# Performance work log

Measured on AMD Instinct MI355X. Metric: run time of the kernel, lower is better.

The kernel has to match this reference:

```python
import jax, jax.numpy as jnp
import numpy as np

HEADS = 8
DIM_HEAD = 64
MAX_POS = 512


def setup_inputs() -> dict:
    key = jax.random.key(0)
    ks = jax.random.split(key, 10)
    b, n, dim, inner = 4, 1024, 512, HEADS * DIM_HEAD
    w = lambda k, shape: jax.random.normal(k, shape, jnp.float32) * 0.02
    return {
        "x": jax.random.normal(ks[0], (b, n, dim, 2), jnp.float32),
        "wq_r": w(ks[1], (dim, inner)),
        "wq_i": w(ks[2], (dim, inner)),
        "wkv_r": w(ks[3], (dim, 2 * inner)),
        "wkv_i": w(ks[4], (dim, 2 * inner)),
        "wo_r": w(ks[5], (inner, dim)),
        "wo_i": w(ks[6], (inner, dim)),
        "bo_r": w(ks[7], (dim,)),
        "bo_i": w(ks[8], (dim,)),
        "rel_emb": w(ks[9], (2 * MAX_POS + 1, DIM_HEAD)),
    }


def _clinear(t, Wr, Wi, br=None, bi=None):
    # complex linear: (a+ib)(Wr+iWi) = (aWr - bWi) + i(bWr + aWi)
    a, b = t[..., 0], t[..., 1]
    r = a @ Wr - b @ Wi
    i = b @ Wr + a @ Wi
    if br is not None:
        r = r + br
        i = i + bi
    return jnp.stack((r, i), axis=-1)


def _split_heads(t, h):
    # [b, n, h*d, 2] -> [b, h, n, d, 2]
    b, n, hd, c = t.shape
    return t.reshape(b, n, h, hd // h, c).transpose(0, 2, 1, 3, 4)


def reference(x, wq_r, wq_i, wkv_r, wkv_i, wo_r, wo_i, bo_r, bo_i, rel_emb):
    b, n = x.shape[0], x.shape[1]
    scale = DIM_HEAD ** (-0.5)

    q = _split_heads(_clinear(x, wq_r, wq_i), HEADS)          # [b,h,n,d,2]
    kv = _clinear(x, wkv_r, wkv_i)                            # [b,n,2*inner,2]
    k_, v_ = jnp.split(kv, 2, axis=-2)
    k = _split_heads(k_, HEADS)
    v = _split_heads(v_, HEADS)

    qr, qi = q[..., 0], q[..., 1]
    kr, ki = k[..., 0], k[..., 1]

    dots_r = (jnp.einsum('bhid,bhjd->bhij', qr, kr)
              - jnp.einsum('bhid,bhjd->bhij', qi, ki)) * scale
    dots_i = (jnp.einsum('bhid,bhjd->bhij', qr, ki)
              + jnp.einsum('bhid,bhjd->bhij', qi, kr)) * scale

    seq = jnp.arange(n)
    dist = jnp.clip(seq[:, None] - seq[None, :], -MAX_POS, MAX_POS) + MAX_POS  # [n,n]
    rel = rel_emb[dist]                                       # [n, n, d]
    dots_r = dots_r + jnp.einsum('bhnd,nrd->bhnr', qr, rel) * scale
    dots_i = dots_i + jnp.einsum('bhnd,nrd->bhnr', qi, rel) * scale

    # magnitude softmax over keys
    attn = jax.nn.softmax(jnp.sqrt(dots_r ** 2 + dots_i ** 2), axis=-1)  # [b,h,i,j]

    vr, vi = v[..., 0], v[..., 1]
    out_r = jnp.einsum('bhij,bhjd->bhid', attn, vr)
    out_i = jnp.einsum('bhij,bhjd->bhid', attn, vi)
    # [b,h,n,d] -> [b,n,h*d]
    out_r = out_r.transpose(0, 2, 1, 3).reshape(b, n, -1)
    out_i = out_i.transpose(0, 2, 1, 3).reshape(b, n, -1)
    out = jnp.stack((out_r, out_i), axis=-1)                  # [b,n,inner,2]

    # to_out (with bias); dropout prob 0 -> identity
    return _clinear(out, wo_r, wo_i, bo_r, bo_i)
```

## Files before the change

kernel.cpp:

```cpp
#include <hip/hip_runtime.h>
#include <hip/hip_bf16.h>


using bf16 = __bf16;
typedef __bf16 bf16x8 __attribute__((ext_vector_type(8)));
typedef float f32x4 __attribute__((ext_vector_type(4)));
typedef unsigned u32x4 __attribute__((ext_vector_type(4)));

#define MFMA16(a, b, c) __builtin_amdgcn_mfma_f32_16x16x32_bf16((a), (b), (c), 0, 0, 0)

__device__ __forceinline__ float ld_in(const void* p, long long i, int f32) {
  return f32 ? ((const float*)p)[i] : (float)((const bf16*)p)[i];
}

__device__ __forceinline__ void gl_lds16(const bf16* g, const bf16* l) {
  __builtin_amdgcn_global_load_lds(
      (const __attribute__((address_space(1))) void*)(unsigned long long)g,
      (__attribute__((address_space(3))) void*)(unsigned int)(unsigned long long)l,
      16, 0, 0);
}

template <int CTRL>
__device__ __forceinline__ float dpp_mv(float v) {
  int s = __builtin_bit_cast(int, v);
  return __builtin_bit_cast(float,
      __builtin_amdgcn_update_dpp(s, s, CTRL, 0xf, 0xf, false));
}
__device__ __forceinline__ float dpp_sum16(float v) {
  v += dpp_mv<0x121>(v);
  v += dpp_mv<0x122>(v);
  v += dpp_mv<0x124>(v);
  v += dpp_mv<0x128>(v);
  return v;
}

__device__ __forceinline__ unsigned pack_bf16(float lo, float hi) {
  unsigned a = (unsigned)__builtin_bit_cast(unsigned short, (bf16)lo);
  unsigned b = (unsigned)__builtin_bit_cast(unsigned short, (bf16)hi);
  return a | (b << 16);
}
__device__ __forceinline__ unsigned pack2h(bf16 lo, bf16 hi) {
  unsigned a = (unsigned)__builtin_bit_cast(unsigned short, lo);
  unsigned b = (unsigned)__builtin_bit_cast(unsigned short, hi);
  return a | (b << 16);
}

__global__ __launch_bounds__(256) void k_diag(float* __restrict__ out, float v) {
  int idx = blockIdx.x * 256 + threadIdx.x;
  if (idx < 4194304) out[idx] = v;
}

__global__ void k_detect_all(
    const unsigned short* p0, const unsigned short* p1, const unsigned short* p2,
    const unsigned short* p3, const unsigned short* p4, const unsigned short* p5,
    const unsigned short* p6, const unsigned short* p7, const unsigned short* p8,
    const unsigned short* p9, int* __restrict__ flags) {
  static const int sizes[10] = {65536, 65536, 65536, 65536, 65536,
                                65536, 65536, 512, 512, 65536};
  const unsigned short* ptrs[10] = {p0, p1, p2, p3, p4, p5, p6, p7, p8, p9};
  __shared__ int cnt;
  if (threadIdx.x == 0) cnt = 0;
  __syncthreads();
  const int which = blockIdx.x;
  const unsigned short* p = ptrs[which];
  const int nhalf = sizes[which];
  const int ns = nhalf < 4096 ? nhalf : 4096;
  const int stp = nhalf / ns;
  int c = 0;
  for (int i = threadIdx.x; i < ns; i += 256) {
    const unsigned u = p[(size_t)i * stp];
    const unsigned e = (u >> 7) & 0xFF;
    if (e == 0xFF || (e < 64 && (u & 0x7FFF) != 0)) ++c;
  }
  atomicAdd(&cnt, c);
  __syncthreads();
  if (threadIdx.x == 0) flags[which] = (cnt > (ns >> 6)) ? 1 : 0;
}

__global__ __launch_bounds__(256) void k_build_all(
    const void* __restrict__ x,
    const void* __restrict__ wq_r, const void* __restrict__ wq_i,
    const void* __restrict__ wkv_r, const void* __restrict__ wkv_i,
    const void* __restrict__ wo_r, const void* __restrict__ wo_i,
    const void* __restrict__ rel,
    bf16* __restrict__ wct, bf16* __restrict__ wot,
    bf16* __restrict__ xd, bf16* __restrict__ rel_c,
    const int* __restrict__ flags) {
  __shared__ float tile[64][65];
  const int bid = blockIdx.x;
  const int t = threadIdx.x;
  if (bid < 1024) {
    const bool is_o = bid >= 768;
    const int lb = is_o ? bid - 768 : bid;
    const int k0 = (lb & 15) * 64;
    const int c0 = (lb >> 4) * 64;
    const int kk0 = k0 & 511;
    const bool hi = k0 >= 512;
    const void* src;
    int f, ld, scol;
    float sgn = 1.f;
    if (is_o) {
      ld = 512;
      if (c0 < 512) { scol = c0;       if (!hi) { src = wo_r; f = flags[5]; } else { src = wo_i; f = flags[6]; sgn = -1.f; } }
      else          { scol = c0 - 512; if (!hi) { src = wo_i; f = flags[6]; } else { src = wo_r; f = flags[5]; } }
    } else {
      if (c0 < 512)       { scol = c0;        ld = 512;  if (!hi) { src = wq_r;  f = flags[1]; } else { src = wq_i;  f = flags[2]; sgn = -1.f; } }
      else if (c0 < 1024) { scol = c0 - 512;  ld = 512;  if (!hi) { src = wq_i;  f = flags[2]; } else { src = wq_r;  f = flags[1]; } }
      else if (c0 < 2048) { scol = c0 - 1024; ld = 1024; if (!hi) { src = wkv_r; f = flags[3]; } else { src = wkv_i; f = flags[4]; sgn = -1.f; } }
      else                { scol = c0 - 2048; ld = 1024; if (!hi) { src = wkv_i; f = flags[4]; } else { src = wkv_r; f = flags[3]; } }
    }
    const int cc = t & 63, rq = t >> 6;
#pragma unroll
    for (int rp = 0; rp < 16; ++rp) {
      const int rr = rp * 4 + rq;
      tile[rr][cc] = sgn * ld_in(src, (long long)(kk0 + rr) * ld + scol + cc, f);
    }
    __syncthreads();
    bf16* dst = is_o ? wot : wct;
    const int cr = t >> 3, kb = (t & 7) * 8;
#pragma unroll
    for (int p = 0; p < 2; ++p) {
      const int c = cr + p * 32;
      bf16x8 v;
#pragma unroll
      for (int e = 0; e < 8; ++e) v[e] = (bf16)tile[kb + e][c];
      *(bf16x8*)(dst + (size_t)(c0 + c) * 1024 + k0 + kb) = v;
    }
  } else if (bid < 9216) {
    const int f = flags[0];
    int idx = (bid - 1024) * 256 + t;
    int m = idx >> 9, j = idx & 511;
    long long base = (long long)m * 1024 + j * 2;
    xd[(size_t)m * 1024 + j] = (bf16)ld_in(x, base, f);
    xd[(size_t)m * 1024 + 512 + j] = (bf16)ld_in(x, base + 1, f);
  } else {
    const int f = flags[9];
    int idx = (bid - 9216) * 256 + t;
    if (idx < 65600) rel_c[idx] = (bf16)ld_in(rel, idx, f);
  }
}

template <int MODE, int BN>
__global__ __launch_bounds__(256) void k_gemm(
    const bf16* __restrict__ A, const bf16* __restrict__ Bt,
    bf16* __restrict__ C, float* __restrict__ Cf,
    const int M, const int N, const int K,
    const void* __restrict__ bias_r, const void* __restrict__ bias_i,
    const int* __restrict__ flags) {
  constexpr int MT = (BN == 128) ? 4 : 2;
  __shared__ __align__(16) bf16 As[128 * 32];
  __shared__ __align__(16) bf16 Bs[BN * 32];
  const int tid = threadIdx.x;
  const int wave = tid >> 6, lane = tid & 63;
  const int lane15 = lane & 15, quad = lane >> 4;
  const int qk0 = quad * 8;
  const int per = gridDim.x >> 3;
  const int s = (blockIdx.x & 7) * per + (blockIdx.x >> 3);
  const int nbx = N / BN;
  const int bm = (s / nbx) * 128, bn = (s % nbx) * BN;
  int wm, wn;
  if constexpr (BN == 128) { wm = (wave >> 1) * 64; wn = (wave & 1) * 64; }
  else                     { wm = wave * 32;        wn = 0; }
  const int sr = lane >> 2;
  const int sc = (lane & 3) * 8;
  f32x4 acc[MT][4];
#pragma unroll
  for (int i = 0; i < MT; ++i)
#pragma unroll
    for (int j = 0; j < 4; ++j) acc[i][j] = (f32x4){0.f, 0.f, 0.f, 0.f};

  for (int k0 = 0; k0 < K; k0 += 32) {
#pragma unroll
    for (int p = 0; p < 2; ++p) {
      const int r0 = p * 64 + wave * 16;
      gl_lds16(A + (size_t)(bm + r0 + sr) * K + k0 + sc, As + r0 * 32);
    }
    if constexpr (BN == 128) {
#pragma unroll
      for (int p = 0; p < 2; ++p) {
        const int r0 = p * 64 + wave * 16;
        gl_lds16(Bt + (size_t)(bn + r0 + sr) * K + k0 + sc, Bs + r0 * 32);
      }
    } else {
      const int r0 = wave * 16;
      gl_lds16(Bt + (size_t)(bn + r0 + sr) * K + k0 + sc, Bs + r0 * 32);
    }
    __syncthreads();
    bf16x8 af[MT], bfr[4];
#pragma unroll
    for (int mt = 0; mt < MT; ++mt) af[mt] = *(const bf16x8*)(As + (wm + mt * 16 + lane15) * 32 + qk0);
#pragma unroll
    for (int nt = 0; nt < 4; ++nt) bfr[nt] = *(const bf16x8*)(Bs + (wn + nt * 16 + lane15) * 32 + qk0);
#pragma unroll
    for (int mt = 0; mt < MT; ++mt)
#pragma unroll
      for (int nt = 0; nt < 4; ++nt) acc[mt][nt] = MFMA16(af[mt], bfr[nt], acc[mt][nt]);
    __syncthreads();
  }
  int fbr = 0, fbi = 0;
  if constexpr (MODE == 1) { fbr = flags[7]; fbi = flags[8]; }
#pragma unroll
  for (int mt = 0; mt < MT; ++mt)
#pragma unroll
    for (int nt = 0; nt < 4; ++nt)
#pragma unroll
      for (int r = 0; r < 4; ++r) {
        const int m = bm + wm + mt * 16 + quad * 4 + r;
        const int n = bn + wn + nt * 16 + lane15;
        float v = acc[mt][nt][r];
        if constexpr (MODE == 0) {
          C[(size_t)m * N + n] = (bf16)v;
        } else {
          const int c = (n < 512) ? n : n - 512;
          v += ld_in((n < 512) ? bias_r : bias_i, c, (n < 512) ? fbr : fbi);
          Cf[(size_t)m * 1024 + c * 2 + ((n < 512) ? 0 : 1)] = v;
        }
      }
}

__global__ __launch_bounds__(256) void k_vt(const bf16* __restrict__ C1,
                                            bf16* __restrict__ vt_r, bf16* __restrict__ vt_i) {
  __shared__ __align__(16) bf16 tr[64][72], ti[64][72];
  const int bid = blockIdx.x, tid = threadIdx.x;
  const int bh = bid >> 4, jt = bid & 15;
  const int b = bh >> 3, h = bh & 7;
  const int j0 = jt * 64;
#pragma unroll
  for (int p = 0; p < 2; ++p) {
    const int j = p * 32 + (tid >> 3);
    const int d0 = (tid & 7) * 8;
    const size_t base = (size_t)(b * 1024 + j0 + j) * 3072 + h * 64 + d0;
    *(bf16x8*)&tr[j][d0] = *(const bf16x8*)(C1 + base + 1536);
    *(bf16x8*)&ti[j][d0] = *(const bf16x8*)(C1 + base + 2560);
  }
  __syncthreads();
#pragma unroll
  for (int p = 0; p < 2; ++p) {
    const int d = p * 32 + (tid >> 3);
    const int p0 = (tid & 7) * 4;
    u32x4 wr, wi;
#pragma unroll
    for (int e = 0; e < 4; ++e) {
      const int pp = p0 + e;
      const int j1 = ((pp >> 4) << 5) + (pp & 15);
      wr[e] = pack2h(tr[j1][d], tr[j1 + 16][d]);
      wi[e] = pack2h(ti[j1][d], ti[j1 + 16][d]);
    }
    const size_t dst = (size_t)(bh * 64 + d) * 512 + jt * 32 + p0;
    *(u32x4*)((unsigned*)vt_r + dst) = wr;
    *(u32x4*)((unsigned*)vt_i + dst) = wi;
  }
}

__device__ __forceinline__ bf16x8 lds_frag72(const bf16* base, int row, int kofs) {
  return *(const bf16x8*)(base + row * 72 + kofs);
}

__global__ __launch_bounds__(256, 2) void k_attn(
    const bf16* __restrict__ C1, const bf16* __restrict__ vt_r, const bf16* __restrict__ vt_i,
    const bf16* __restrict__ rel, bf16* __restrict__ Oc) {
  __shared__ __align__(16) bf16 kr_s[64 * 72];
  __shared__ __align__(16) bf16 ki_s[64 * 72];
  __shared__ __align__(16) bf16 vtr_s[64 * 72];
  __shared__ __align__(16) bf16 vti_s[64 * 72];
  __shared__ unsigned Gt32[4][1360];

  const int tid = threadIdx.x;
  const int wave = tid >> 6, lane = tid & 63;
  const int lane15 = lane & 15, quad = lane >> 4;
  const int qk0 = quad * 8;
  const int bid0 = blockIdx.x;
  const int bid = (bid0 & 7) * 64 + (bid0 >> 3);
  const int bh = bid >> 4, it = bid & 15;
  const int b = bh >> 3, h = bh & 7;
  const int i0 = it * 64;
  const int tq = tid >> 3;
  const int tc = (tid & 7) * 8;

  unsigned* const Gw = &Gt32[wave][0];

  const size_t qbase = (size_t)(b * 1024 + i0 + wave * 16 + lane15) * 3072 + h * 64;
  bf16x8 aqr[2], aqi[2], aqin[2];
  aqr[0] = *(const bf16x8*)(C1 + qbase + qk0);
  aqr[1] = *(const bf16x8*)(C1 + qbase + 32 + qk0);
  aqi[0] = *(const bf16x8*)(C1 + qbase + 512 + qk0);
  aqi[1] = *(const bf16x8*)(C1 + qbase + 512 + 32 + qk0);
#pragma unroll
  for (int c = 0; c < 2; ++c)
#pragma unroll
    for (int e = 0; e < 8; ++e) aqin[c][e] = (bf16)(-(float)aqi[c][e]);

  f32x4 o_r[4], o_i[4];
#pragma unroll
  for (int dt = 0; dt < 4; ++dt) { o_r[dt] = (f32x4){0.f,0.f,0.f,0.f}; o_i[dt] = (f32x4){0.f,0.f,0.f,0.f}; }
  float l_st[4] = {0.f, 0.f, 0.f, 0.f};

  bf16x8 pKr[2], pKi[2], pVr[2], pVi[2];
  auto issueKV = [&](int jtn) {
    const int j0 = jtn * 64;
#pragma unroll
    for (int p = 0; p < 2; ++p) {
      const int row = p * 32 + tq;
      const size_t gbase = (size_t)(b * 1024 + j0 + row) * 3072 + h * 64 + tc;
      pKr[p] = *(const bf16x8*)(C1 + gbase + 1024);
      pKi[p] = *(const bf16x8*)(C1 + gbase + 2048);
      const size_t vbase = (size_t)(bh * 64 + row) * 1024 + j0 + tc;
      pVr[p] = *(const bf16x8*)(vt_r + vbase);
      pVi[p] = *(const bf16x8*)(vt_i + vbase);
    }
  };

  bf16x8 rb0[5], rb1[5];
  auto loadR = [&](int jtn) {
    const int t0w = 449 + i0 - jtn * 64 + wave * 16;
#pragma unroll
    for (int g = 0; g < 5; ++g) {
      int trw = t0w + g * 16 + lane15;
      trw = trw < 0 ? 0 : (trw > 1024 ? 1024 : trw);
      const bf16* rp = rel + (size_t)trw * 64;
      rb0[g] = *(const bf16x8*)(rp + qk0);
      rb1[g] = *(const bf16x8*)(rp + 32 + qk0);
    }
  };

  issueKV(0);
  loadR(0);
  for (int jt = 0; jt < 16; ++jt) {
#pragma unroll
    for (int p = 0; p < 2; ++p) {
      const int row = p * 32 + tq;
      *(bf16x8*)(kr_s + row * 72 + tc) = pKr[p];
      *(bf16x8*)(ki_s + row * 72 + tc) = pKi[p];
      *(bf16x8*)(vtr_s + row * 72 + tc) = pVr[p];
      *(bf16x8*)(vti_s + row * 72 + tc) = pVi[p];
    }
    __syncthreads();
    if (jt < 15) issueKV(jt + 1);

    f32x4 s_r[4], s_i[4];
#pragma unroll
    for (int ct = 0; ct < 4; ++ct) { s_r[ct] = (f32x4){0.f,0.f,0.f,0.f}; s_i[ct] = (f32x4){0.f,0.f,0.f,0.f}; }
    __builtin_amdgcn_s_setprio(1);
#pragma unroll
    for (int ct = 0; ct < 4; ++ct) {
      const int krow = ct * 16 + lane15;
      bf16x8 bkr0 = lds_frag72(kr_s, krow, qk0), bkr1 = lds_frag72(kr_s, krow, 32 + qk0);
      bf16x8 bki0 = lds_frag72(ki_s, krow, qk0), bki1 = lds_frag72(ki_s, krow, 32 + qk0);
      s_r[ct] = MFMA16(aqr[0], bkr0, s_r[ct]);
      s_r[ct] = MFMA16(aqr[1], bkr1, s_r[ct]);
      s_r[ct] = MFMA16(aqin[0], bki0, s_r[ct]);
      s_r[ct] = MFMA16(aqin[1], bki1, s_r[ct]);
      s_i[ct] = MFMA16(aqr[0], bki0, s_i[ct]);
      s_i[ct] = MFMA16(aqr[1], bki1, s_i[ct]);
      s_i[ct] = MFMA16(aqi[0], bkr0, s_i[ct]);
      s_i[ct] = MFMA16(aqi[1], bkr1, s_i[ct]);
    }
    __builtin_amdgcn_s_setprio(0);

#pragma unroll
    for (int g = 0; g < 5; ++g) {
      f32x4 gr = (f32x4){0.f,0.f,0.f,0.f}, gi = (f32x4){0.f,0.f,0.f,0.f};
      gr = MFMA16(aqr[0], rb0[g], gr);
      gr = MFMA16(aqr[1], rb1[g], gr);
      gi = MFMA16(aqi[0], rb0[g], gi);
      gi = MFMA16(aqi[1], rb1[g], gi);
      const int trow = (g * 16 + lane15) * 17;
#pragma unroll
      for (int r = 0; r < 4; ++r)
        Gw[trow + quad * 4 + r] = pack_bf16(gr[r], gi[r]);
    }

    if (jt < 15) loadR(jt + 1);

    float mag[4][4];
#pragma unroll
    for (int ct = 0; ct < 4; ++ct) {
      const int jj = ct * 16 + lane15;
#pragma unroll
      for (int r = 0; r < 4; ++r) {
        const int ii = quad * 4 + r;
        const unsigned gv = Gw[(ii - jj + 63) * 17 + ii];
        const float gr = __builtin_bit_cast(float, gv << 16);
        const float gi = __builtin_bit_cast(float, gv & 0xffff0000u);
        const float dr = s_r[ct][r] + gr;
        const float di = s_i[ct][r] + gi;
        mag[ct][r] = fminf(0.125f * sqrtf(dr * dr + di * di), 80.f);
      }
    }
#pragma unroll
    for (int r = 0; r < 4; ++r) {
      const int ii = quad * 4 + r;
      float pv[4];
#pragma unroll
      for (int ct = 0; ct < 4; ++ct) pv[ct] = __expf(mag[ct][r]);
      l_st[r] += (pv[0] + pv[1]) + (pv[2] + pv[3]);
      Gw[ii * 36 + lane15]      = pack_bf16(pv[0], pv[1]);
      Gw[ii * 36 + 16 + lane15] = pack_bf16(pv[2], pv[3]);
    }

    bf16x8 ap0 = *(const bf16x8*)(Gw + lane15 * 36 + quad * 4);
    bf16x8 ap1 = *(const bf16x8*)(Gw + lane15 * 36 + 16 + quad * 4);
    __builtin_amdgcn_s_setprio(1);
#pragma unroll
    for (int dt = 0; dt < 4; ++dt) {
      const int vrow = dt * 16 + lane15;
      bf16x8 bv0 = lds_frag72(vtr_s, vrow, qk0), bv1 = lds_frag72(vtr_s, vrow, 32 + qk0);
      o_r[dt] = MFMA16(ap0, bv0, o_r[dt]);
      o_r[dt] = MFMA16(ap1, bv1, o_r[dt]);
      bv0 = lds_frag72(vti_s, vrow, qk0);
      bv1 = lds_frag72(vti_s, vrow, 32 + qk0);
      o_i[dt] = MFMA16(ap0, bv0, o_i[dt]);
      o_i[dt] = MFMA16(ap1, bv1, o_i[dt]);
    }
    __builtin_amdgcn_s_setprio(0);
    __syncthreads();
  }

  const size_t obase = (size_t)(b * 1024 + i0 + wave * 16) * 1024 + h * 64;
#pragma unroll
  for (int r = 0; r < 4; ++r) {
    const float inv = 1.0f / dpp_sum16(l_st[r]);
    const int ii = quad * 4 + r;
#pragma unroll
    for (int dt = 0; dt < 4; ++dt) {
      Oc[obase + (size_t)ii * 1024 + dt * 16 + lane15] = (bf16)(o_r[dt][r] * inv);
      Oc[obase + (size_t)ii * 1024 + 512 + dt * 16 + lane15] = (bf16)(o_i[dt][r] * inv);
    }
  }
}

extern "C" void kernel_launch(void* const* d_in, const int* in_sizes, int n_in,
                              void* d_out, int out_size, void* d_ws, size_t ws_size,
                              hipStream_t stream) {
  float* out = (float*)d_out;

  if (n_in != 10) { k_diag<<<16384, 256, 0, stream>>>(out, 300000.f); return; }
  if (out_size != 4194304) { k_diag<<<16384, 256, 0, stream>>>(out, 400000.f); return; }
  static const int dict_sizes[10] = {4194304, 262144, 262144, 524288, 524288,
                                     262144, 262144, 512, 512, 65600};
  for (int i = 0; i < 10; ++i) {
    if (in_sizes[i] != dict_sizes[i]) { k_diag<<<16384, 256, 0, stream>>>(out, 200000.f); return; }
  }
  const size_t NEED = 50462888;
  if (ws_size < NEED) { k_diag<<<16384, 256, 0, stream>>>(out, 100000.f); return; }

  const void* x     = d_in[0];
  const void* wq_r  = d_in[1];
  const void* wq_i  = d_in[2];
  const void* wkv_r = d_in[3];
  const void* wkv_i = d_in[4];
  const void* wo_r  = d_in[5];
  const void* wo_i  = d_in[6];
  const void* bo_r  = d_in[7];
  const void* bo_i  = d_in[8];
  const void* rel   = d_in[9];

  char* ws = (char*)d_ws;
  bf16* C1   = (bf16*)(ws);
  bf16* Xd   = (bf16*)(ws + 25165824);
  bf16* Vtr  = (bf16*)(ws + 25165824);
  bf16* Vti  = (bf16*)(ws + 29360128);
  bf16* Oc   = (bf16*)(ws + 33554432);
  bf16* WcT  = (bf16*)(ws + 41943040);
  bf16* WoT  = (bf16*)(ws + 48234496);
  bf16* relc = (bf16*)(ws + 50331648);
  int*  flags= (int*)(ws + 50462848);

  k_detect_all<<<10, 256, 0, stream>>>(
      (const unsigned short*)x, (const unsigned short*)wq_r, (const unsigned short*)wq_i,
      (const unsigned short*)wkv_r, (const unsigned short*)wkv_i, (const unsigned short*)wo_r,
      (const unsigned short*)wo_i, (const unsigned short*)bo_r, (const unsigned short*)bo_i,
      (const unsigned short*)rel, flags);

  k_build_all<<<9473, 256, 0, stream>>>(x, wq_r, wq_i, wkv_r, wkv_i, wo_r, wo_i, rel,
                                        WcT, WoT, Xd, relc, flags);

  k_gemm<0, 128><<<768, 256, 0, stream>>>(Xd, WcT, C1, nullptr, 4096, 3072, 1024,
                                          nullptr, nullptr, flags);
  k_vt<<<512, 256, 0, stream>>>(C1, Vtr, Vti);
  k_attn<<<512, 256, 0, stream>>>(C1, Vtr, Vti, relc, Oc);
  k_gemm<1, 64><<<512, 256, 0, stream>>>(Oc, WoT, nullptr, out, 4096, 1024, 1024,
                                         bo_r, bo_i, flags);
}
```

Baseline: 238.6 us.

## Split attention key loop across two wave groups and load V fragments from global

The attention block grows to 512 threads, with two groups of four waves. Each group handles alternating 64-key tiles for the same query rows, and the partial outputs and row sums are combined through LDS at the end. V fragments are now read directly from global memory into registers instead of being staged in shared memory, which cuts LDS traffic and footprint. This doubles the waves per query tile and adds a final reduction. The direct global V reads may hurt latency hiding, and the larger block may change occupancy.

```diff
diff --git a/kernel.cpp b/kernel.cpp
--- a/kernel.cpp
+++ b/kernel.cpp
@@ -256,17 +256,17 @@
   return *(const bf16x8*)(base + row * 72 + kofs);
 }
 
-__global__ __launch_bounds__(256, 2) void k_attn(
+__global__ __launch_bounds__(512, 4) void k_attn(
     const bf16* __restrict__ C1, const bf16* __restrict__ vt_r, const bf16* __restrict__ vt_i,
     const bf16* __restrict__ rel, bf16* __restrict__ Oc) {
-  __shared__ __align__(16) bf16 kr_s[64 * 72];
-  __shared__ __align__(16) bf16 ki_s[64 * 72];
-  __shared__ __align__(16) bf16 vtr_s[64 * 72];
-  __shared__ __align__(16) bf16 vti_s[64 * 72];
-  __shared__ unsigned Gt32[4][1360];
+  __shared__ __align__(16) bf16 k_s[2][2][64 * 72];
+  __shared__ unsigned Gt32[8][1360];
 
   const int tid = threadIdx.x;
-  const int wave = tid >> 6, lane = tid & 63;
+  const int wave = tid >> 6;
+  const int grp = wave >> 2;
+  const int w4 = wave & 3;
+  const int lane = tid & 63;
   const int lane15 = lane & 15, quad = lane >> 4;
   const int qk0 = quad * 8;
   const int bid0 = blockIdx.x;
@@ -274,12 +274,15 @@
   const int bh = bid >> 4, it = bid & 15;
   const int b = bh >> 3, h = bh & 7;
   const int i0 = it * 64;
-  const int tq = tid >> 3;
-  const int tc = (tid & 7) * 8;
+  const int tid256 = tid & 255;
+  const int tq = tid256 >> 3;
+  const int tc = (tid256 & 7) * 8;
 
   unsigned* const Gw = &Gt32[wave][0];
-
-  const size_t qbase = (size_t)(b * 1024 + i0 + wave * 16 + lane15) * 3072 + h * 64;
+  bf16* const krs = &k_s[grp][0][0];
+  bf16* const kis = &k_s[grp][1][0];
+
+  const size_t qbase = (size_t)(b * 1024 + i0 + w4 * 16 + lane15) * 3072 + h * 64;
   bf16x8 aqr[2], aqi[2], aqin[2];
   aqr[0] = *(const bf16x8*)(C1 + qbase + qk0);
   aqr[1] = *(const bf16x8*)(C1 + qbase + 32 + qk0);
@@ -293,10 +296,10 @@
   f32x4 o_r[4], o_i[4];
 #pragma unroll
   for (int dt = 0; dt < 4; ++dt) { o_r[dt] = (f32x4){0.f,0.f,0.f,0.f}; o_i[dt] = (f32x4){0.f,0.f,0.f,0.f}; }
-  float l_st[4] = {0.f, 0.f, 0.f, 0.f};
-
-  bf16x8 pKr[2], pKi[2], pVr[2], pVi[2];
-  auto issueKV = [&](int jtn) {
+  f32x4 l_st = (f32x4){0.f, 0.f, 0.f, 0.f};
+
+  bf16x8 pKr[2], pKi[2];
+  auto issueK = [&](int jtn) {
     const int j0 = jtn * 64;
 #pragma unroll
     for (int p = 0; p < 2; ++p) {
@@ -304,15 +307,12 @@
       const size_t gbase = (size_t)(b * 1024 + j0 + row) * 3072 + h * 64 + tc;
       pKr[p] = *(const bf16x8*)(C1 + gbase + 1024);
       pKi[p] = *(const bf16x8*)(C1 + gbase + 2048);
-      const size_t vbase = (size_t)(bh * 64 + row) * 1024 + j0 + tc;
-      pVr[p] = *(const bf16x8*)(vt_r + vbase);
-      pVi[p] = *(const bf16x8*)(vt_i + vbase);
     }
   };
 
   bf16x8 rb0[5], rb1[5];
   auto loadR = [&](int jtn) {
-    const int t0w = 449 + i0 - jtn * 64 + wave * 16;
+    const int t0w = 449 + i0 - jtn * 64 + w4 * 16;
 #pragma unroll
     for (int g = 0; g < 5; ++g) {
       int trw = t0w + g * 16 + lane15;
@@ -323,19 +323,26 @@
     }
   };
 
-  issueKV(0);
-  loadR(0);
-  for (int jt = 0; jt < 16; ++jt) {
+  issueK(grp);
+  loadR(grp);
+  for (int k = 0; k < 8; ++k) {
+    const int jt = 2 * k + grp;
 #pragma unroll
     for (int p = 0; p < 2; ++p) {
       const int row = p * 32 + tq;
-      *(bf16x8*)(kr_s + row * 72 + tc) = pKr[p];
-      *(bf16x8*)(ki_s + row * 72 + tc) = pKi[p];
-      *(bf16x8*)(vtr_s + row * 72 + tc) = pVr[p];
-      *(bf16x8*)(vti_s + row * 72 + tc) = pVi[p];
+      *(bf16x8*)(krs + row * 72 + tc) = pKr[p];
+      *(bf16x8*)(kis + row * 72 + tc) = pKi[p];
     }
     __syncthreads();
-    if (jt < 15) issueKV(jt + 1);
+    if (k < 7) issueK(2 * (k + 1) + grp);
+
+    bf16x8 vr0[4], vr1[4];
+#pragma unroll
+    for (int dt = 0; dt < 4; ++dt) {
+      const size_t vb = (size_t)(bh * 64 + dt * 16 + lane15) * 1024 + jt * 64;
+      vr0[dt] = *(const bf16x8*)(vt_r + vb + qk0);
+      vr1[dt] = *(const bf16x8*)(vt_r + vb + 32 + qk0);
+    }
 
     f32x4 s_r[4], s_i[4];
 #pragma unroll
@@ -344,8 +351,8 @@
 #pragma unroll
     for (int ct = 0; ct < 4; ++ct) {
       const int krow = ct * 16 + lane15;
-      bf16x8 bkr0 = lds_frag72(kr_s, krow, qk0), bkr1 = lds_frag72(kr_s, krow, 32 + qk0);
-      bf16x8 bki0 = lds_frag72(ki_s, krow, qk0), bki1 = lds_frag72(ki_s, krow, 32 + qk0);
+      bf16x8 bkr0 = lds_frag72(krs, krow, qk0), bkr1 = lds_frag72(krs, krow, 32 + qk0);
+      bf16x8 bki0 = lds_frag72(kis, krow, qk0), bki1 = lds_frag72(kis, krow, 32 + qk0);
       s_r[ct] = MFMA16(aqr[0], bkr0, s_r[ct]);
       s_r[ct] = MFMA16(aqr[1], bkr1, s_r[ct]);
       s_r[ct] = MFMA16(aqin[0], bki0, s_r[ct]);
@@ -357,6 +364,14 @@
     }
     __builtin_amdgcn_s_setprio(0);
 
+    bf16x8 vi0[4], vi1[4];
+#pragma unroll
+    for (int dt = 0; dt < 4; ++dt) {
+      const size_t vb = (size_t)(bh * 64 + dt * 16 + lane15) * 1024 + jt * 64;
+      vi0[dt] = *(const bf16x8*)(vt_i + vb + qk0);
+      vi1[dt] = *(const bf16x8*)(vt_i + vb + 32 + qk0);
+    }
+
 #pragma unroll
     for (int g = 0; g < 5; ++g) {
       f32x4 gr = (f32x4){0.f,0.f,0.f,0.f}, gi = (f32x4){0.f,0.f,0.f,0.f};
@@ -370,7 +385,7 @@
         Gw[trow + quad * 4 + r] = pack_bf16(gr[r], gi[r]);
     }
 
-    if (jt < 15) loadR(jt + 1);
+    if (k < 7) loadR(2 * (k + 1) + grp);
 
     float mag[4][4];
 #pragma unroll
@@ -398,33 +413,51 @@
       Gw[ii * 36 + 16 + lane15] = pack_bf16(pv[2], pv[3]);
     }
 
-    bf16x8 ap0 = *(const bf16x8*)(Gw + lane15 * 36 + quad * 4);
-    bf16x8 ap1 = *(const bf16x8*)(Gw + lane15 * 36 + 16 + quad * 4);
+    bf16x8 ap0 = *(const bf16x8*)((const bf16*)Gw + lane15 * 72 + quad * 8);
+    bf16x8 ap1 = *(const bf16x8*)((const bf16*)Gw + lane15 * 72 + 32 + quad * 8);
     __builtin_amdgcn_s_setprio(1);
 #pragma unroll
     for (int dt = 0; dt < 4; ++dt) {
-      const int vrow = dt * 16 + lane15;
-      bf16x8 bv0 = lds_frag72(vtr_s, vrow, qk0), bv1 = lds_frag72(vtr_s, vrow, 32 + qk0);
-      o_r[dt] = MFMA16(ap0, bv0, o_r[dt]);
-      o_r[dt] = MFMA16(ap1, bv1, o_r[dt]);
-      bv0 = lds_frag72(vti_s, vrow, qk0);
-      bv1 = lds_frag72(vti_s, vrow, 32 + qk0);
-      o_i[dt] = MFMA16(ap0, bv0, o_i[dt]);
-      o_i[dt] = MFMA16(ap1, bv1, o_i[dt]);
+      o_r[dt] = MFMA16(ap0, vr0[dt], o_r[dt]);
+      o_r[dt] = MFMA16(ap1, vr1[dt], o_r[dt]);
+    }
+#pragma unroll
+    for (int dt = 0; dt < 4; ++dt) {
+      o_i[dt] = MFMA16(ap0, vi0[dt], o_i[dt]);
+      o_i[dt] = MFMA16(ap1, vi1[dt], o_i[dt]);
     }
     __builtin_amdgcn_s_setprio(0);
     __syncthreads();
   }
 
-  const size_t obase = (size_t)(b * 1024 + i0 + wave * 16) * 1024 + h * 64;
-#pragma unroll
-  for (int r = 0; r < 4; ++r) {
-    const float inv = 1.0f / dpp_sum16(l_st[r]);
-    const int ii = quad * 4 + r;
+  float* cb = (float*)&k_s[0][0][0];
+  const int base = tid256 * 36;
+  if (grp == 1) {
 #pragma unroll
     for (int dt = 0; dt < 4; ++dt) {
-      Oc[obase + (size_t)ii * 1024 + dt * 16 + lane15] = (bf16)(o_r[dt][r] * inv);
-      Oc[obase + (size_t)ii * 1024 + 512 + dt * 16 + lane15] = (bf16)(o_i[dt][r] * inv);
+      *(f32x4*)(cb + base + dt * 8) = o_r[dt];
+      *(f32x4*)(cb + base + dt * 8 + 4) = o_i[dt];
+    }
+    *(f32x4*)(cb + base + 32) = l_st;
+  }
+  __syncthreads();
+  if (grp == 0) {
+#pragma unroll
+    for (int dt = 0; dt < 4; ++dt) {
+      o_r[dt] += *(const f32x4*)(cb + base + dt * 8);
+      o_i[dt] += *(const f32x4*)(cb + base + dt * 8 + 4);
+    }
+    l_st += *(const f32x4*)(cb + base + 32);
+    const size_t obase = (size_t)(b * 1024 + i0 + w4 * 16) * 1024 + h * 64;
+#pragma unroll
+    for (int r = 0; r < 4; ++r) {
+      const float inv = 1.0f / dpp_sum16(l_st[r]);
+      const int ii = quad * 4 + r;
+#pragma unroll
+      for (int dt = 0; dt < 4; ++dt) {
+        Oc[obase + (size_t)ii * 1024 + dt * 16 + lane15] = (bf16)(o_r[dt][r] * inv);
+        Oc[obase + (size_t)ii * 1024 + 512 + dt * 16 + lane15] = (bf16)(o_i[dt][r] * inv);
+      }
     }
   }
 }
@@ -478,7 +511,7 @@
   k_gemm<0, 128><<<768, 256, 0, stream>>>(Xd, WcT, C1, nullptr, 4096, 3072, 1024,
                                           nullptr, nullptr, flags);
   k_vt<<<512, 256, 0, stream>>>(C1, Vtr, Vti);
-  k_attn<<<512, 256, 0, stream>>>(C1, Vtr, Vti, relc, Oc);
+  k_attn<<<512, 512, 0, stream>>>(C1, Vtr, Vti, relc, Oc);
   k_gemm<1, 64><<<512, 256, 0, stream>>>(Oc, WoT, nullptr, out, 4096, 1024, 1024,
                                          bo_r, bo_i, flags);
 }
```

Result: slower. 481.0 us (+101.6%).

## Pre-swizzle V into MFMA fragment layout and read directly from global; swizzle GEMM LDS

Applied to the files above, without the earlier changes.

The V-transpose kernel now writes V in an MFMA-fragment-ready order so the attention kernel loads B operands for the PV product straight from global memory into registers, dropping two LDS tiles and their stores. This frees LDS, so occupancy is raised to 3 blocks per CU. The rel-embedding loads are moved into the loop body without prefetch, and the barrier placement changes. The GEMM kernel doubles its K tile to 64 and uses an XOR-swizzled LDS layout to avoid bank conflicts. The risk is more global-load latency exposed in the attention inner loop, since V and rel are no longer prefetched a tile ahead.

```diff
diff --git a/kernel.cpp b/kernel.cpp
--- a/kernel.cpp
+++ b/kernel.cpp
@@ -148,12 +148,11 @@
     const void* __restrict__ bias_r, const void* __restrict__ bias_i,
     const int* __restrict__ flags) {
   constexpr int MT = (BN == 128) ? 4 : 2;
-  __shared__ __align__(16) bf16 As[128 * 32];
-  __shared__ __align__(16) bf16 Bs[BN * 32];
+  __shared__ __align__(16) bf16 As[128 * 64];
+  __shared__ __align__(16) bf16 Bs[BN * 64];
   const int tid = threadIdx.x;
   const int wave = tid >> 6, lane = tid & 63;
   const int lane15 = lane & 15, quad = lane >> 4;
-  const int qk0 = quad * 8;
   const int per = gridDim.x >> 3;
   const int s = (blockIdx.x & 7) * per + (blockIdx.x >> 3);
   const int nbx = N / BN;
@@ -161,40 +160,50 @@
   int wm, wn;
   if constexpr (BN == 128) { wm = (wave >> 1) * 64; wn = (wave & 1) * 64; }
   else                     { wm = wave * 32;        wn = 0; }
-  const int sr = lane >> 2;
-  const int sc = (lane & 3) * 8;
+  const int sr = lane >> 3;
+  const int scs = ((lane & 7) ^ sr) * 8;
+  const int s7 = lane15 & 7;
   f32x4 acc[MT][4];
 #pragma unroll
   for (int i = 0; i < MT; ++i)
 #pragma unroll
     for (int j = 0; j < 4; ++j) acc[i][j] = (f32x4){0.f, 0.f, 0.f, 0.f};
 
-  for (int k0 = 0; k0 < K; k0 += 32) {
-#pragma unroll
-    for (int p = 0; p < 2; ++p) {
-      const int r0 = p * 64 + wave * 16;
-      gl_lds16(A + (size_t)(bm + r0 + sr) * K + k0 + sc, As + r0 * 32);
+  for (int k0 = 0; k0 < K; k0 += 64) {
+#pragma unroll
+    for (int p = 0; p < 4; ++p) {
+      const int g = wave * 4 + p;
+      gl_lds16(A + (size_t)(bm + g * 8 + sr) * K + k0 + scs, As + g * 512);
     }
     if constexpr (BN == 128) {
 #pragma unroll
-      for (int p = 0; p < 2; ++p) {
-        const int r0 = p * 64 + wave * 16;
-        gl_lds16(Bt + (size_t)(bn + r0 + sr) * K + k0 + sc, Bs + r0 * 32);
+      for (int p = 0; p < 4; ++p) {
+        const int g = wave * 4 + p;
+        gl_lds16(Bt + (size_t)(bn + g * 8 + sr) * K + k0 + scs, Bs + g * 512);
       }
     } else {
-      const int r0 = wave * 16;
-      gl_lds16(Bt + (size_t)(bn + r0 + sr) * K + k0 + sc, Bs + r0 * 32);
+#pragma unroll
+      for (int p = 0; p < 2; ++p) {
+        const int g = wave * 2 + p;
+        gl_lds16(Bt + (size_t)(bn + g * 8 + sr) * K + k0 + scs, Bs + g * 512);
+      }
     }
     __syncthreads();
-    bf16x8 af[MT], bfr[4];
-#pragma unroll
-    for (int mt = 0; mt < MT; ++mt) af[mt] = *(const bf16x8*)(As + (wm + mt * 16 + lane15) * 32 + qk0);
-#pragma unroll
-    for (int nt = 0; nt < 4; ++nt) bfr[nt] = *(const bf16x8*)(Bs + (wn + nt * 16 + lane15) * 32 + qk0);
-#pragma unroll
-    for (int mt = 0; mt < MT; ++mt)
-#pragma unroll
-      for (int nt = 0; nt < 4; ++nt) acc[mt][nt] = MFMA16(af[mt], bfr[nt], acc[mt][nt]);
+#pragma unroll
+    for (int kk = 0; kk < 2; ++kk) {
+      const int go = ((kk * 4 + quad) ^ s7) * 8;
+      bf16x8 af[MT], bfr[4];
+#pragma unroll
+      for (int mt = 0; mt < MT; ++mt)
+        af[mt] = *(const bf16x8*)(As + (wm + mt * 16 + lane15) * 64 + go);
+#pragma unroll
+      for (int nt = 0; nt < 4; ++nt)
+        bfr[nt] = *(const bf16x8*)(Bs + (wn + nt * 16 + lane15) * 64 + go);
+#pragma unroll
+      for (int mt = 0; mt < MT; ++mt)
+#pragma unroll
+        for (int nt = 0; nt < 4; ++nt) acc[mt][nt] = MFMA16(af[mt], bfr[nt], acc[mt][nt]);
+    }
     __syncthreads();
   }
   int fbr = 0, fbi = 0;
@@ -234,21 +243,21 @@
     *(bf16x8*)&ti[j][d0] = *(const bf16x8*)(C1 + base + 2560);
   }
   __syncthreads();
-#pragma unroll
-  for (int p = 0; p < 2; ++p) {
-    const int d = p * 32 + (tid >> 3);
-    const int p0 = (tid & 7) * 4;
+  const int dt = tid >> 6, l = tid & 63;
+  const int q = l >> 4, m = l & 15;
+  const int d = dt * 16 + m;
+  const size_t base = ((size_t)(bh * 16 + jt) << 11) + (size_t)dt * 512 + l * 4;
+#pragma unroll
+  for (int half = 0; half < 2; ++half) {
     u32x4 wr, wi;
 #pragma unroll
     for (int e = 0; e < 4; ++e) {
-      const int pp = p0 + e;
-      const int j1 = ((pp >> 4) << 5) + (pp & 15);
+      const int j1 = half * 32 + q * 4 + e;
       wr[e] = pack2h(tr[j1][d], tr[j1 + 16][d]);
       wi[e] = pack2h(ti[j1][d], ti[j1 + 16][d]);
     }
-    const size_t dst = (size_t)(bh * 64 + d) * 512 + jt * 32 + p0;
-    *(u32x4*)((unsigned*)vt_r + dst) = wr;
-    *(u32x4*)((unsigned*)vt_i + dst) = wi;
+    *(u32x4*)((unsigned*)vt_r + base + half * 256) = wr;
+    *(u32x4*)((unsigned*)vt_i + base + half * 256) = wi;
   }
 }
 
@@ -256,13 +265,11 @@
   return *(const bf16x8*)(base + row * 72 + kofs);
 }
 
-__global__ __launch_bounds__(256, 2) void k_attn(
+__global__ __launch_bounds__(256, 3) void k_attn(
     const bf16* __restrict__ C1, const bf16* __restrict__ vt_r, const bf16* __restrict__ vt_i,
     const bf16* __restrict__ rel, bf16* __restrict__ Oc) {
   __shared__ __align__(16) bf16 kr_s[64 * 72];
   __shared__ __align__(16) bf16 ki_s[64 * 72];
-  __shared__ __align__(16) bf16 vtr_s[64 * 72];
-  __shared__ __align__(16) bf16 vti_s[64 * 72];
   __shared__ unsigned Gt32[4][1360];
 
   const int tid = threadIdx.x;
@@ -293,10 +300,10 @@
   f32x4 o_r[4], o_i[4];
 #pragma unroll
   for (int dt = 0; dt < 4; ++dt) { o_r[dt] = (f32x4){0.f,0.f,0.f,0.f}; o_i[dt] = (f32x4){0.f,0.f,0.f,0.f}; }
-  float l_st[4] = {0.f, 0.f, 0.f, 0.f};
-
-  bf16x8 pKr[2], pKi[2], pVr[2], pVi[2];
-  auto issueKV = [&](int jtn) {
+  f32x4 l_st = (f32x4){0.f, 0.f, 0.f, 0.f};
+
+  bf16x8 pKr[2], pKi[2];
+  auto issueK = [&](int jtn) {
     const int j0 = jtn * 64;
 #pragma unroll
     for (int p = 0; p < 2; ++p) {
@@ -304,38 +311,44 @@
       const size_t gbase = (size_t)(b * 1024 + j0 + row) * 3072 + h * 64 + tc;
       pKr[p] = *(const bf16x8*)(C1 + gbase + 1024);
       pKi[p] = *(const bf16x8*)(C1 + gbase + 2048);
-      const size_t vbase = (size_t)(bh * 64 + row) * 1024 + j0 + tc;
-      pVr[p] = *(const bf16x8*)(vt_r + vbase);
-      pVi[p] = *(const bf16x8*)(vt_i + vbase);
     }
   };
 
-  bf16x8 rb0[5], rb1[5];
-  auto loadR = [&](int jtn) {
-    const int t0w = 449 + i0 - jtn * 64 + wave * 16;
-#pragma unroll
-    for (int g = 0; g < 5; ++g) {
-      int trw = t0w + g * 16 + lane15;
-      trw = trw < 0 ? 0 : (trw > 1024 ? 1024 : trw);
-      const bf16* rp = rel + (size_t)trw * 64;
-      rb0[g] = *(const bf16x8*)(rp + qk0);
-      rb1[g] = *(const bf16x8*)(rp + 32 + qk0);
-    }
-  };
-
-  issueKV(0);
-  loadR(0);
+  issueK(0);
   for (int jt = 0; jt < 16; ++jt) {
+    bf16x8 rb0[5], rb1[5];
+    {
+      const int t0w = 449 + i0 - jt * 64 + wave * 16;
+#pragma unroll
+      for (int g = 0; g < 5; ++g) {
+        int trw = t0w + g * 16 + lane15;
+        trw = trw < 0 ? 0 : (trw > 1024 ? 1024 : trw);
+        const bf16* rp = rel + (size_t)trw * 64;
+        rb0[g] = *(const bf16x8*)(rp + qk0);
+        rb1[g] = *(const bf16x8*)(rp + 32 + qk0);
+      }
+    }
 #pragma unroll
     for (int p = 0; p < 2; ++p) {
       const int row = p * 32 + tq;
       *(bf16x8*)(kr_s + row * 72 + tc) = pKr[p];
       *(bf16x8*)(ki_s + row * 72 + tc) = pKi[p];
-      *(bf16x8*)(vtr_s + row * 72 + tc) = pVr[p];
-      *(bf16x8*)(vti_s + row * 72 + tc) = pVi[p];
     }
     __syncthreads();
-    if (jt < 15) issueKV(jt + 1);
+    if (jt < 15) issueK(jt + 1);
+
+#pragma unroll
+    for (int g = 0; g < 5; ++g) {
+      f32x4 gr = (f32x4){0.f,0.f,0.f,0.f}, gi = (f32x4){0.f,0.f,0.f,0.f};
+      gr = MFMA16(aqr[0], rb0[g], gr);
+      gr = MFMA16(aqr[1], rb1[g], gr);
+      gi = MFMA16(aqi[0], rb0[g], gi);
+      gi = MFMA16(aqi[1], rb1[g], gi);
+      const int trow = (g * 16 + lane15) * 17;
+#pragma unroll
+      for (int r = 0; r < 4; ++r)
+        Gw[trow + quad * 4 + r] = pack_bf16(gr[r], gi[r]);
+    }
 
     f32x4 s_r[4], s_i[4];
 #pragma unroll
@@ -356,21 +369,16 @@
       s_i[ct] = MFMA16(aqi[1], bkr1, s_i[ct]);
     }
     __builtin_amdgcn_s_setprio(0);
-
-#pragma unroll
-    for (int g = 0; g < 5; ++g) {
-      f32x4 gr = (f32x4){0.f,0.f,0.f,0.f}, gi = (f32x4){0.f,0.f,0.f,0.f};
-      gr = MFMA16(aqr[0], rb0[g], gr);
-      gr = MFMA16(aqr[1], rb1[g], gr);
-      gi = MFMA16(aqi[0], rb0[g], gi);
-      gi = MFMA16(aqi[1], rb1[g], gi);
-      const int trow = (g * 16 + lane15) * 17;
-#pragma unroll
-      for (int r = 0; r < 4; ++r)
-        Gw[trow + quad * 4 + r] = pack_bf16(gr[r], gi[r]);
-    }
-
-    if (jt < 15) loadR(jt + 1);
+    __syncthreads();
+
+    const unsigned* vbr = (const unsigned*)vt_r + ((size_t)(bh * 16 + jt) << 11);
+    const unsigned* vbi = (const unsigned*)vt_i + ((size_t)(bh * 16 + jt) << 11);
+    bf16x8 vr0[4], vr1[4];
+#pragma unroll
+    for (int dt = 0; dt < 4; ++dt) {
+      vr0[dt] = *(const bf16x8*)(vbr + dt * 512 + lane * 4);
+      vr1[dt] = *(const bf16x8*)(vbr + dt * 512 + 256 + lane * 4);
+    }
 
     float mag[4][4];
 #pragma unroll
@@ -398,22 +406,27 @@
       Gw[ii * 36 + 16 + lane15] = pack_bf16(pv[2], pv[3]);
     }
 
-    bf16x8 ap0 = *(const bf16x8*)(Gw + lane15 * 36 + quad * 4);
-    bf16x8 ap1 = *(const bf16x8*)(Gw + lane15 * 36 + 16 + quad * 4);
+    bf16x8 vi0[4], vi1[4];
+#pragma unroll
+    for (int dt = 0; dt < 4; ++dt) {
+      vi0[dt] = *(const bf16x8*)(vbi + dt * 512 + lane * 4);
+      vi1[dt] = *(const bf16x8*)(vbi + dt * 512 + 256 + lane * 4);
+    }
+
+    bf16x8 ap0 = *(const bf16x8*)((const bf16*)Gw + lane15 * 72 + quad * 8);
+    bf16x8 ap1 = *(const bf16x8*)((const bf16*)Gw + lane15 * 72 + 32 + quad * 8);
     __builtin_amdgcn_s_setprio(1);
 #pragma unroll
     for (int dt = 0; dt < 4; ++dt) {
-      const int vrow = dt * 16 + lane15;
-      bf16x8 bv0 = lds_frag72(vtr_s, vrow, qk0), bv1 = lds_frag72(vtr_s, vrow, 32 + qk0);
-      o_r[dt] = MFMA16(ap0, bv0, o_r[dt]);
-      o_r[dt] = MFMA16(ap1, bv1, o_r[dt]);
-      bv0 = lds_frag72(vti_s, vrow, qk0);
-      bv1 = lds_frag72(vti_s, vrow, 32 + qk0);
-      o_i[dt] = MFMA16(ap0, bv0, o_i[dt]);
-      o_i[dt] = MFMA16(ap1, bv1, o_i[dt]);
+      o_r[dt] = MFMA16(ap0, vr0[dt], o_r[dt]);
+      o_r[dt] = MFMA16(ap1, vr1[dt], o_r[dt]);
+    }
+#pragma unroll
+    for (int dt = 0; dt < 4; ++dt) {
+      o_i[dt] = MFMA16(ap0, vi0[dt], o_i[dt]);
+      o_i[dt] = MFMA16(ap1, vi1[dt], o_i[dt]);
     }
     __builtin_amdgcn_s_setprio(0);
-    __syncthreads();
   }
 
   const size_t obase = (size_t)(b * 1024 + i0 + wave * 16) * 1024 + h * 64;
```

After: 295.8 us. 1.24x slower.
